# Performance work log

Measured on AMD Instinct MI355X. Metric: run time of the kernel, lower is better.

The kernel has to match this reference:

```python
import jax, jax.numpy as jnp
import numpy as np

TEMPERATURE = 0.5
EPS = 1e-8  # torch F.cosine_similarity eps


def _neg_mask_indices(two_b):
    """Static row/col indices replicating sim[mask].view(2B, -1).
    Mask excludes the diagonal and the (i, B+i)/(B+i, i) positive pairs,
    leaving exactly 2B-2 entries per row, extracted in row-major order."""
    b = two_b // 2
    mask = np.ones((two_b, two_b), dtype=bool)
    np.fill_diagonal(mask, False)
    i = np.arange(b)
    mask[i, b + i] = False
    mask[b + i, i] = False
    rows, cols = np.nonzero(mask)
    return rows.reshape(two_b, two_b - 2), cols.reshape(two_b, two_b - 2)


def setup_inputs() -> dict:
    key = jax.random.key(0)
    k1, k2 = jax.random.split(key)
    two_b, d = 8192, 128
    embeddings = jax.random.normal(k1, (two_b, d), dtype=jnp.float32)
    labels = jax.random.randint(k2, (two_b,), 0, two_b - 2)
    return {"embeddings": embeddings, "labels": labels}


def reference(embeddings, labels):
    two_b = embeddings.shape[0]
    # cosine similarity via normalize + matmul (same math as the broadcast
    # F.cosine_similarity, without the O(N^2*D) intermediate)
    norms = jnp.linalg.norm(embeddings, axis=1)  # [2B]
    sim = (embeddings @ embeddings.T) / jnp.maximum(norms[:, None] * norms[None, :], EPS)
    sim = sim / TEMPERATURE  # [2B, 2B]
    rows, cols = _neg_mask_indices(two_b)
    logits = sim[rows, cols]  # [2B, 2B-2]
    # CrossEntropyLoss(reduction='sum') then / (2B)
    logz = jax.nn.logsumexp(logits, axis=1)  # [2B]
    picked = jnp.take_along_axis(logits, labels[:, None].astype(jnp.int32), axis=1)[:, 0]
    loss = jnp.sum(logz - picked) / two_b
    return loss
```

## Files before the change

### kernel.cpp

```cpp
#include <hip/hip_runtime.h>
#include <hip/hip_bf16.h>


typedef __bf16 bf16x8 __attribute__((ext_vector_type(8)));
typedef float floatx4 __attribute__((ext_vector_type(4)));

#define TWO_B 8192
#define B_HALF 4096
#define D 128
#define INV_T 2.0f
#define FIXED_MAX 2.0f
#define C_EXP 2.885390081777927f

#if defined(__has_builtin) && __has_builtin(__builtin_amdgcn_exp2f)
#define EXP2F(x) __builtin_amdgcn_exp2f(x)
#else
#define EXP2F(x) exp2f(x)
#endif
#if defined(__has_builtin) && __has_builtin(__builtin_amdgcn_logf)
#define LOG2F(x) __builtin_amdgcn_logf(x)
#else
#define LOG2F(x) log2f(x)
#endif

__device__ inline void load16_lds(const __bf16* g, __bf16* l) {
    __builtin_amdgcn_global_load_lds(
        (const __attribute__((address_space(1))) unsigned int*)g,
        (__attribute__((address_space(3))) unsigned int*)l, 16, 0, 0);
}

__global__ void k_prep(const float* __restrict__ emb,
                       const int* __restrict__ labels,
                       __bf16* __restrict__ nb,
                       float* __restrict__ picked,
                       float* __restrict__ l_arr) {
    int wv   = threadIdx.x >> 6;
    int lane = threadIdx.x & 63;
    int i = blockIdx.x * 4 + wv;
    const float2* e2 = reinterpret_cast<const float2*>(emb + (size_t)i * D);
    float2 v = e2[lane];
    float ssi = v.x * v.x + v.y * v.y;
    int p = i ^ B_HALF;
    int a = min(i, p), b = max(i, p);
    int l = labels[i];
    int c = l + (l >= a);
    c += (c >= b);
    const float2* ec2 = reinterpret_cast<const float2*>(emb + (size_t)c * D);
    float2 u = ec2[lane];
    float dot = v.x * u.x + v.y * u.y;
    float ssc = u.x * u.x + u.y * u.y;
#pragma unroll
    for (int off = 32; off >= 1; off >>= 1) {
        ssi += __shfl_xor(ssi, off, 64);
        dot += __shfl_xor(dot, off, 64);
        ssc += __shfl_xor(ssc, off, 64);
    }
    float rn = rsqrtf(fmaxf(ssi, 1e-16f));
    union { __bf16 h[2]; unsigned int uu; } pk;
    pk.h[0] = (__bf16)(v.x * rn);
    pk.h[1] = (__bf16)(v.y * rn);
    reinterpret_cast<unsigned int*>(nb)[i * 64 + lane] = pk.uu;
    if (lane == 0)
        picked[i] = dot / fmaxf(sqrtf(ssi * ssc), 1e-8f) * INV_T;
    if (blockIdx.x < TWO_B / 256) l_arr[blockIdx.x * 256 + threadIdx.x] = 0.f;
}

__global__ __launch_bounds__(256, 4) void k_gemm(const __bf16* __restrict__ nb,
                                                 float* __restrict__ l_arr) {
    __shared__ __bf16 lds[16384];

    const int bi = blockIdx.x;
    const int g  = blockIdx.y;

    const int lane = threadIdx.x & 63;
    const int w    = threadIdx.x >> 6;
    const int m    = lane & 15;
    const int quad = lane >> 4;
    const int row0 = bi * 128 + w * 32;

    bf16x8 a0[4], a1[4];
#pragma unroll
    for (int kc = 0; kc < 4; ++kc) {
        a0[kc] = *reinterpret_cast<const bf16x8*>(
            nb + (size_t)(row0 + m) * D + kc * 32 + quad * 8);
        a1[kc] = *reinterpret_cast<const bf16x8*>(
            nb + (size_t)(row0 + 16 + m) * D + kc * 32 + quad * 8);
    }
    asm volatile("" : "+v"(a0[0]), "+v"(a0[1]), "+v"(a0[2]), "+v"(a0[3]),
                      "+v"(a1[0]), "+v"(a1[1]), "+v"(a1[2]), "+v"(a1[3]));

    float l0[4] = {0.f, 0.f, 0.f, 0.f};
    float l1[4] = {0.f, 0.f, 0.f, 0.f};
    const int i0 = row0 + quad * 4;

    bool first = true;
#pragma unroll
    for (int si = 0; si < 2; ++si) {
        const int by = g + si * 17;
        if (by > 32) continue;
        if (by == 32 && bi >= 32) continue;
        const int bj = (bi + by) & 63;
        const int C0 = bj * 128;
        const bool isdiag = (by == 0);
        const bool bmask = isdiag || (by == 32);

        if (!first) __syncthreads();
        first = false;

        {
            const __bf16* gp = nb + (size_t)(C0 + m) * D + w * 32 + quad * 8;
#pragma unroll
            for (int j = 0; j < 8; ++j)
                load16_lds(gp + (size_t)j * 16 * D, &lds[j * 2048 + w * 512]);
        }
        __syncthreads();

        float csum[8];
#pragma unroll
        for (int grp = 0; grp < 2; ++grp) {
            floatx4 acc0[4] = {{0.f,0.f,0.f,0.f},{0.f,0.f,0.f,0.f},
                               {0.f,0.f,0.f,0.f},{0.f,0.f,0.f,0.f}};
            floatx4 acc1[4] = {{0.f,0.f,0.f,0.f},{0.f,0.f,0.f,0.f},
                               {0.f,0.f,0.f,0.f},{0.f,0.f,0.f,0.f}};
#pragma unroll
            for (int kc = 0; kc < 4; ++kc) {
                const bf16x8 a0k = a0[kc], a1k = a1[kc];
#pragma unroll
                for (int s = 0; s < 4; ++s) {
                    bf16x8 b = *reinterpret_cast<const bf16x8*>(
                        &lds[((grp * 4 + s) * 4 + kc) * 512 + lane * 8]);
                    acc0[s] = __builtin_amdgcn_mfma_f32_16x16x32_bf16(a0k, b, acc0[s], 0, 0, 0);
                    acc1[s] = __builtin_amdgcn_mfma_f32_16x16x32_bf16(a1k, b, acc1[s], 0, 0, 0);
                }
            }
#pragma unroll
            for (int s = 0; s < 4; ++s) {
                const int jj = C0 + (grp * 4 + s) * 16 + m;
                float cs = 0.f;
                if (bmask) {
#pragma unroll
                    for (int r = 0; r < 4; ++r) {
                        float e0 = EXP2F(fmaf(acc0[s][r], C_EXP, -C_EXP));
                        float e1 = EXP2F(fmaf(acc1[s][r], C_EXP, -C_EXP));
                        if (((jj ^ (i0 + r)) & ~B_HALF) == 0) e0 = 0.f;
                        if (((jj ^ (i0 + 16 + r)) & ~B_HALF) == 0) e1 = 0.f;
                        l0[r] += e0;
                        l1[r] += e1;
                        cs += e0 + e1;
                    }
                } else {
#pragma unroll
                    for (int r = 0; r < 4; ++r) {
                        float e0 = EXP2F(fmaf(acc0[s][r], C_EXP, -C_EXP));
                        float e1 = EXP2F(fmaf(acc1[s][r], C_EXP, -C_EXP));
                        l0[r] += e0;
                        l1[r] += e1;
                        cs += e0 + e1;
                    }
                }
                cs += __shfl_xor(cs, 16, 64);
                cs += __shfl_xor(cs, 32, 64);
                csum[grp * 4 + s] = cs;
            }
        }

        if (!isdiag) {
            __syncthreads();
            float* ldsf = reinterpret_cast<float*>(lds);
            if (quad == 0) {
#pragma unroll
                for (int sub = 0; sub < 8; ++sub)
                    ldsf[w * 128 + sub * 16 + m] = csum[sub];
            }
            __syncthreads();
            if (threadIdx.x < 128) {
                float t = ldsf[threadIdx.x] + ldsf[128 + threadIdx.x] +
                          ldsf[256 + threadIdx.x] + ldsf[384 + threadIdx.x];
                atomicAdd(&l_arr[C0 + threadIdx.x], t);
            }
        }
    }

#pragma unroll
    for (int r = 0; r < 4; ++r) {
        float s = l0[r];
        s += __shfl_xor(s, 1, 64);
        s += __shfl_xor(s, 2, 64);
        s += __shfl_xor(s, 4, 64);
        s += __shfl_xor(s, 8, 64);
        if (m == 0) atomicAdd(&l_arr[i0 + r], s);
    }
#pragma unroll
    for (int r = 0; r < 4; ++r) {
        float s = l1[r];
        s += __shfl_xor(s, 1, 64);
        s += __shfl_xor(s, 2, 64);
        s += __shfl_xor(s, 4, 64);
        s += __shfl_xor(s, 8, 64);
        if (m == 0) atomicAdd(&l_arr[i0 + 16 + r], s);
    }
}

__global__ void k_final(const float* __restrict__ l_arr,
                        const float* __restrict__ picked,
                        float* __restrict__ out) {
    __shared__ float sred[16];
    float s = 0.f;
#pragma unroll
    for (int k = 0; k < TWO_B / 1024; ++k) {
        int i = threadIdx.x + k * 1024;
        s += FIXED_MAX + LOG2F(l_arr[i]) * 0.6931471805599453f - picked[i];
    }
#pragma unroll
    for (int off = 32; off >= 1; off >>= 1) s += __shfl_xor(s, off, 64);
    if ((threadIdx.x & 63) == 0) sred[threadIdx.x >> 6] = s;
    __syncthreads();
    if (threadIdx.x == 0) {
        float t = 0.f;
#pragma unroll
        for (int k = 0; k < 16; ++k) t += sred[k];
        out[0] = t * (1.0f / TWO_B);
    }
}

extern "C" void kernel_launch(void* const* d_in, const int* in_sizes, int n_in,
                              void* d_out, int out_size, void* d_ws, size_t ws_size,
                              hipStream_t stream) {
    const float* emb    = (const float*)d_in[0];
    const int*   labels = (const int*)d_in[1];
    char* ws = (char*)d_ws;
    float*  l_arr  = (float*)ws;
    float*  picked = (float*)(ws + 32768);
    __bf16* nb     = (__bf16*)(ws + 65536);
    float*  out    = (float*)d_out;

    k_prep<<<TWO_B / 4, 256, 0, stream>>>(emb, labels, nb, picked, l_arr);
    dim3 g2(64, 17);
    k_gemm<<<g2, 256, 0, stream>>>(nb, l_arr);
    k_final<<<1, 1024, 0, stream>>>(l_arr, picked, out);
}
```

Measured before the change: 83.09 us.

## Fuse final reduction into GEMM via per-row completion counters

Removes the separate single-block final kernel by tracking per-row contribution counts with atomics in the GEMM kernel. The block that completes a row computes its log-sum-exp term and adds it to a global accumulator, and the last finished row writes the output. This saves one kernel launch and its serial tail, at the cost of extra atomics, vmcnt drains, and ordering assumptions about memory visibility across blocks.

After: 107.4 us. 1.29x slower.

```diff
diff --git a/kernel.cpp b/kernel.cpp
--- a/kernel.cpp
+++ b/kernel.cpp
@@ -11,6 +11,7 @@
 #define INV_T 2.0f
 #define FIXED_MAX 2.0f
 #define C_EXP 2.885390081777927f
+#define LN2 0.6931471805599453f
 
 #if defined(__has_builtin) && __has_builtin(__builtin_amdgcn_exp2f)
 #define EXP2F(x) __builtin_amdgcn_exp2f(x)
@@ -23,17 +24,38 @@
 #define LOG2F(x) log2f(x)
 #endif
 
+#define VM_DRAIN() asm volatile("s_waitcnt vmcnt(0)" ::: "memory")
+
 __device__ inline void load16_lds(const __bf16* g, __bf16* l) {
     __builtin_amdgcn_global_load_lds(
         (const __attribute__((address_space(1))) unsigned int*)g,
         (__attribute__((address_space(3))) unsigned int*)l, 16, 0, 0);
 }
 
+__device__ inline void finalize_row(int i, float* __restrict__ l_arr,
+                                    const float* __restrict__ picked,
+                                    float* __restrict__ accum,
+                                    unsigned int* __restrict__ rows_done,
+                                    float* __restrict__ out) {
+    float lv = atomicAdd(&l_arr[i], 0.0f);
+    float term = FIXED_MAX + LOG2F(lv) * LN2 - picked[i];
+    atomicAdd(accum, term);
+    VM_DRAIN();
+    unsigned int gd = atomicAdd(rows_done, 1u);
+    if (gd == TWO_B - 1) {
+        float tot = atomicAdd(accum, 0.0f);
+        out[0] = tot * (1.0f / TWO_B);
+    }
+}
+
 __global__ void k_prep(const float* __restrict__ emb,
                        const int* __restrict__ labels,
                        __bf16* __restrict__ nb,
                        float* __restrict__ picked,
-                       float* __restrict__ l_arr) {
+                       float* __restrict__ l_arr,
+                       int* __restrict__ l_cnt,
+                       float* __restrict__ accum,
+                       unsigned int* __restrict__ rows_done) {
     int wv   = threadIdx.x >> 6;
     int lane = threadIdx.x & 63;
     int i = blockIdx.x * 4 + wv;
@@ -62,11 +84,20 @@
     reinterpret_cast<unsigned int*>(nb)[i * 64 + lane] = pk.uu;
     if (lane == 0)
         picked[i] = dot / fmaxf(sqrtf(ssi * ssc), 1e-8f) * INV_T;
-    if (blockIdx.x < TWO_B / 256) l_arr[blockIdx.x * 256 + threadIdx.x] = 0.f;
+    if (blockIdx.x < 32)
+        l_arr[blockIdx.x * 256 + threadIdx.x] = 0.f;
+    else if (blockIdx.x < 64)
+        l_cnt[(blockIdx.x - 32) * 256 + threadIdx.x] = 0;
+    if (blockIdx.x == 0 && threadIdx.x == 0) { accum[0] = 0.f; rows_done[0] = 0u; }
 }
 
 __global__ __launch_bounds__(256, 4) void k_gemm(const __bf16* __restrict__ nb,
-                                                 float* __restrict__ l_arr) {
+                                                 float* __restrict__ l_arr,
+                                                 int* __restrict__ l_cnt,
+                                                 const float* __restrict__ picked,
+                                                 float* __restrict__ accum,
+                                                 unsigned int* __restrict__ rows_done,
+                                                 float* __restrict__ out) {
     __shared__ __bf16 lds[16384];
 
     const int bi = blockIdx.x;
@@ -92,6 +123,9 @@
     float l0[4] = {0.f, 0.f, 0.f, 0.f};
     float l1[4] = {0.f, 0.f, 0.f, 0.f};
     const int i0 = row0 + quad * 4;
+
+    int   ccol[2] = {-1, -1};
+    float cval[2] = {0.f, 0.f};
 
     bool first = true;
 #pragma unroll
@@ -177,10 +211,13 @@
                 float t = ldsf[threadIdx.x] + ldsf[128 + threadIdx.x] +
                           ldsf[256 + threadIdx.x] + ldsf[384 + threadIdx.x];
                 atomicAdd(&l_arr[C0 + threadIdx.x], t);
-            }
-        }
-    }
-
+                ccol[si] = C0 + threadIdx.x;
+                cval[si] = t;
+            }
+        }
+    }
+
+    float rsum[8];
 #pragma unroll
     for (int r = 0; r < 4; ++r) {
         float s = l0[r];
@@ -188,38 +225,48 @@
         s += __shfl_xor(s, 2, 64);
         s += __shfl_xor(s, 4, 64);
         s += __shfl_xor(s, 8, 64);
-        if (m == 0) atomicAdd(&l_arr[i0 + r], s);
-    }
-#pragma unroll
-    for (int r = 0; r < 4; ++r) {
-        float s = l1[r];
-        s += __shfl_xor(s, 1, 64);
-        s += __shfl_xor(s, 2, 64);
-        s += __shfl_xor(s, 4, 64);
-        s += __shfl_xor(s, 8, 64);
-        if (m == 0) atomicAdd(&l_arr[i0 + 16 + r], s);
-    }
-}
-
-__global__ void k_final(const float* __restrict__ l_arr,
-                        const float* __restrict__ picked,
-                        float* __restrict__ out) {
-    __shared__ float sred[16];
-    float s = 0.f;
-#pragma unroll
-    for (int k = 0; k < TWO_B / 1024; ++k) {
-        int i = threadIdx.x + k * 1024;
-        s += FIXED_MAX + LOG2F(l_arr[i]) * 0.6931471805599453f - picked[i];
-    }
-#pragma unroll
-    for (int off = 32; off >= 1; off >>= 1) s += __shfl_xor(s, off, 64);
-    if ((threadIdx.x & 63) == 0) sred[threadIdx.x >> 6] = s;
-    __syncthreads();
-    if (threadIdx.x == 0) {
-        float t = 0.f;
-#pragma unroll
-        for (int k = 0; k < 16; ++k) t += sred[k];
-        out[0] = t * (1.0f / TWO_B);
+        rsum[r] = s;
+        float t = l1[r];
+        t += __shfl_xor(t, 1, 64);
+        t += __shfl_xor(t, 2, 64);
+        t += __shfl_xor(t, 4, 64);
+        t += __shfl_xor(t, 8, 64);
+        rsum[4 + r] = t;
+    }
+    if (m == 0) {
+#pragma unroll
+        for (int k = 0; k < 8; ++k)
+            atomicAdd(&l_arr[i0 + (k >> 2) * 16 + (k & 3)], rsum[k]);
+    }
+
+    VM_DRAIN();
+    int rdn[8];
+    if (m == 0) {
+#pragma unroll
+        for (int k = 0; k < 8; ++k)
+            rdn[k] = atomicAdd(&l_cnt[i0 + (k >> 2) * 16 + (k & 3)], 1);
+    }
+    int cdn[2] = {0, 0};
+#pragma unroll
+    for (int si = 0; si < 2; ++si)
+        if (ccol[si] >= 0) cdn[si] = atomicAdd(&l_cnt[ccol[si]], 1);
+
+    if (m == 0) {
+#pragma unroll
+        for (int k = 0; k < 8; ++k) {
+            int i = i0 + (k >> 2) * 16 + (k & 3);
+            int need = 48 + (i >= B_HALF);
+            if (rdn[k] == need - 1)
+                finalize_row(i, l_arr, picked, accum, rows_done, out);
+        }
+    }
+#pragma unroll
+    for (int si = 0; si < 2; ++si) {
+        if (ccol[si] >= 0) {
+            int need = 48 + (ccol[si] >= B_HALF);
+            if (cdn[si] == need - 1)
+                finalize_row(ccol[si], l_arr, picked, accum, rows_done, out);
+        }
     }
 }
 
@@ -229,13 +276,17 @@
     const float* emb    = (const float*)d_in[0];
     const int*   labels = (const int*)d_in[1];
     char* ws = (char*)d_ws;
-    float*  l_arr  = (float*)ws;
-    float*  picked = (float*)(ws + 32768);
-    __bf16* nb     = (__bf16*)(ws + 65536);
-    float*  out    = (float*)d_out;
-
-    k_prep<<<TWO_B / 4, 256, 0, stream>>>(emb, labels, nb, picked, l_arr);
+    float*        l_arr     = (float*)ws;
+    float*        picked    = (float*)(ws + 32768);
+    int*          l_cnt     = (int*)(ws + 65536);
+    float*        accum     = (float*)(ws + 98304);
+    unsigned int* rows_done = (unsigned int*)(ws + 98308);
+    __bf16*       nb        = (__bf16*)(ws + 98560);
+    float*        out       = (float*)d_out;
+
+    k_prep<<<TWO_B / 4, 256, 0, stream>>>(emb, labels, nb, picked, l_arr,
+                                          l_cnt, accum, rows_done);
     dim3 g2(64, 17);
-    k_gemm<<<g2, 256, 0, stream>>>(nb, l_arr);
-    k_final<<<1, 1024, 0, stream>>>(l_arr, picked, out);
-}
+    k_gemm<<<g2, 256, 0, stream>>>(nb, l_arr, l_cnt, picked, accum,
+                                   rows_done, out);
+}
```
